# Optimization experiments

Measured on AMD Instinct MI355X. Metric: run time of the kernel, lower is better.

Reference implementation:

```python
import jax, jax.numpy as jnp
import numpy as np

N_NODES = 40000
N_EDGES = 640000
IN_CH = 128
HID_CH = 128
BN_EPS = 1e-5


def setup_inputs() -> dict:
    key = jax.random.key(0)
    k_x, k_ei, k_w, k_g = jax.random.split(key, 4)
    x = jax.random.normal(k_x, (N_NODES, IN_CH), dtype=jnp.float32)
    edge_index = jax.random.randint(k_ei, (2, N_EDGES), 0, N_NODES, dtype=jnp.int32)
    # Glorot init for GCNConv weight, zero bias (PyG defaults)
    limit = float(np.sqrt(6.0 / (IN_CH + HID_CH)))
    W = jax.random.uniform(k_w, (IN_CH, HID_CH), dtype=jnp.float32, minval=-limit, maxval=limit)
    b = jnp.zeros((HID_CH,), dtype=jnp.float32)
    gamma = jnp.ones((HID_CH,), dtype=jnp.float32)
    beta = jnp.zeros((HID_CH,), dtype=jnp.float32)
    return {"x": x, "edge_index": edge_index, "W": W, "b": b, "gamma": gamma, "beta": beta}


def reference(x, edge_index, W, b, gamma, beta):
    N = x.shape[0]
    src, dst = edge_index[0], edge_index[1]

    # --- GCNConv: h = x @ W, symmetric-normalized aggregation with self-loops ---
    h = x @ W  # [N, H]
    ones = jnp.ones((src.shape[0],), dtype=x.dtype)
    deg = jax.ops.segment_sum(ones, dst, num_segments=N) + 1.0  # +1 for self-loop
    dinv = jax.lax.rsqrt(deg)  # deg >= 1 always
    norm = dinv[src] * dinv[dst]  # [E]
    msg = h[src] * norm[:, None]  # [E, H] gather
    agg = jax.ops.segment_sum(msg, dst, num_segments=N)  # scatter-add
    agg = agg + h * (dinv * dinv)[:, None]  # self-loop contribution
    out = agg + b  # bias added after aggregation (PyG GCNConv)

    # --- BatchNorm1d (training mode: batch stats, biased variance) ---
    mean = jnp.mean(out, axis=0)
    var = jnp.mean((out - mean) ** 2, axis=0)
    out = gamma * (out - mean) * jax.lax.rsqrt(var + BN_EPS) + beta

    # --- ReLU (dropout is a no-op in eval) ---
    return jax.nn.relu(out)
```

## Files before the change

### kernel.cpp

```cpp
#include <hip/hip_runtime.h>

#define N_NODES 40000
#define N_EDGES 640000
#define CH 128
#define BN_EPS 1e-5f
#define CAP 64
#define MM_ROWS 32
#define MM_BLOCKS (N_NODES / MM_ROWS)
#define FILL_BLOCKS ((N_EDGES + 255) / 256)


__device__ __forceinline__ float bf_lo(unsigned u) { return __uint_as_float(u << 16); }
__device__ __forceinline__ float bf_hi(unsigned u) { return __uint_as_float(u & 0xffff0000u); }
__device__ __forceinline__ unsigned short f2bf(float f) {
    unsigned u = __float_as_uint(f);
    unsigned r = 0x7fffu + ((u >> 16) & 1u);
    return (unsigned short)((u + r) >> 16);
}
__device__ __forceinline__ unsigned pack2bf(float a, float b) {
    return (unsigned)f2bf(a) | ((unsigned)f2bf(b) << 16);
}

__global__ __launch_bounds__(256) void mm_fill_kernel(const float* __restrict__ x,
                                                      const float* __restrict__ W,
                                                      unsigned short* __restrict__ hbf,
                                                      const int* __restrict__ src,
                                                      const int* __restrict__ dst,
                                                      int* __restrict__ cnt,
                                                      unsigned short* __restrict__ bucket16) {
    __shared__ unsigned Wsb[CH * CH / 2];
    __shared__ unsigned xsb[CH * 16];
    int t = threadIdx.x;
    int bb = blockIdx.x;
    if (bb % 3 != 0) {
        int fillIdx = bb - (bb / 3) - 1;
        int base = cnt[N_NODES];
        int e = fillIdx * 256 + t;
        if (e < N_EDGES) {
            int d = dst[e];
            int slot = atomicAdd(&cnt[d], 1) - base;
            if (slot < CAP) bucket16[d * CAP + slot] = (unsigned short)src[e];
        }
        return;
    }
    int mmIdx = bb / 3;
    for (int i = t; i < CH * CH / 4; i += 256) {
        float4 w = ((const float4*)W)[i];
        uint2 p;
        p.x = pack2bf(w.x, w.y);
        p.y = pack2bf(w.z, w.w);
        ((uint2*)Wsb)[i] = p;
    }
    size_t row0 = (size_t)mmIdx * MM_ROWS;
    {
        int p = t >> 4;
        int k4a = t & 15;
#pragma unroll
        for (int kk = 0; kk < 2; ++kk) {
            int k4 = k4a + kk * 16;
            float4 xa = ((const float4*)(x + (row0 + p) * CH))[k4];
            float4 xb = ((const float4*)(x + (row0 + p + 16) * CH))[k4];
            xsb[(k4 * 4 + 0) * 16 + p] = pack2bf(xa.x, xb.x);
            xsb[(k4 * 4 + 1) * 16 + p] = pack2bf(xa.y, xb.y);
            xsb[(k4 * 4 + 2) * 16 + p] = pack2bf(xa.z, xb.z);
            xsb[(k4 * 4 + 3) * 16 + p] = pack2bf(xa.w, xb.w);
        }
    }
    __syncthreads();
    int ch4 = t & 31;
    int rg = t >> 5;
    float4 accA = {0,0,0,0}, accB = {0,0,0,0}, accC = {0,0,0,0}, accD = {0,0,0,0};
#pragma unroll 8
    for (int k = 0; k < CH; ++k) {
        uint2 wp = ((const uint2*)Wsb)[k * 32 + ch4];
        unsigned xpa = xsb[k * 16 + rg];
        unsigned xpb = xsb[k * 16 + rg + 8];
        float w0 = bf_lo(wp.x), w1 = bf_hi(wp.x), w2 = bf_lo(wp.y), w3 = bf_hi(wp.y);
        float xa0 = bf_lo(xpa), xa1 = bf_hi(xpa);
        float xb0 = bf_lo(xpb), xb1 = bf_hi(xpb);
        accA.x += xa0 * w0; accA.y += xa0 * w1; accA.z += xa0 * w2; accA.w += xa0 * w3;
        accB.x += xa1 * w0; accB.y += xa1 * w1; accB.z += xa1 * w2; accB.w += xa1 * w3;
        accC.x += xb0 * w0; accC.y += xb0 * w1; accC.z += xb0 * w2; accC.w += xb0 * w3;
        accD.x += xb1 * w0; accD.y += xb1 * w1; accD.z += xb1 * w2; accD.w += xb1 * w3;
    }
    uint2 o;
    o.x = pack2bf(accA.x, accA.y); o.y = pack2bf(accA.z, accA.w);
    ((uint2*)(hbf + (row0 + rg) * CH))[ch4] = o;
    o.x = pack2bf(accB.x, accB.y); o.y = pack2bf(accB.z, accB.w);
    ((uint2*)(hbf + (row0 + rg + 16) * CH))[ch4] = o;
    o.x = pack2bf(accC.x, accC.y); o.y = pack2bf(accC.z, accC.w);
    ((uint2*)(hbf + (row0 + rg + 8) * CH))[ch4] = o;
    o.x = pack2bf(accD.x, accD.y); o.y = pack2bf(accD.z, accD.w);
    ((uint2*)(hbf + (row0 + rg + 24) * CH))[ch4] = o;
}

__global__ __launch_bounds__(256) void aggregate_kernel(const unsigned short* __restrict__ bucket16,
                                                        const int* __restrict__ cnt,
                                                        const unsigned short* __restrict__ hbf,
                                                        const float* __restrict__ b,
                                                        float* __restrict__ out,
                                                        float* __restrict__ sums32) {
    __shared__ float bsum[CH], bsq[CH];
    int t = threadIdx.x;
    if (t < CH) { bsum[t] = 0.0f; bsq[t] = 0.0f; }
    __syncthreads();
    int base = cnt[N_NODES];
    int n = blockIdx.x * 4 + (t >> 6);
    int lane = t & 63;
    int quarter = lane >> 4;
    int ql = lane & 15;
    int cn = cnt[n] - base;
    int m = cn < CAP ? cn : CAP;
    float dn = rsqrtf((float)cn + 1.0f);
    const uint4* h4 = (const uint4*)hbf;
    unsigned sx_pre = (lane < m) ? (unsigned)bucket16[n * CAP + lane] : 0u;
    float a0 = 0, a1 = 0, a2 = 0, a3 = 0, a4 = 0, a5 = 0, a6 = 0, a7 = 0;
    for (int jj = 0; jj < m; jj += 16) {
        int e = jj + quarter * 4;
        unsigned sx0 = (unsigned)__shfl((int)sx_pre, e, 64);
        unsigned sx1 = (unsigned)__shfl((int)sx_pre, e + 1, 64);
        unsigned sx2 = (unsigned)__shfl((int)sx_pre, e + 2, 64);
        unsigned sx3 = (unsigned)__shfl((int)sx_pre, e + 3, 64);
        int c0g = cnt[sx0];
        int c1g = cnt[sx1];
        int c2g = cnt[sx2];
        int c3g = cnt[sx3];
        uint4 r0 = h4[(size_t)sx0 * 16 + ql];
        uint4 r1 = h4[(size_t)sx1 * 16 + ql];
        uint4 r2 = h4[(size_t)sx2 * 16 + ql];
        uint4 r3 = h4[(size_t)sx3 * 16 + ql];
        float d0 = (e     < m) ? rsqrtf((float)(c0g - base) + 1.0f) : 0.0f;
        float d1 = (e + 1 < m) ? rsqrtf((float)(c1g - base) + 1.0f) : 0.0f;
        float d2 = (e + 2 < m) ? rsqrtf((float)(c2g - base) + 1.0f) : 0.0f;
        float d3 = (e + 3 < m) ? rsqrtf((float)(c3g - base) + 1.0f) : 0.0f;
        a0 += bf_lo(r0.x) * d0; a1 += bf_hi(r0.x) * d0;
        a2 += bf_lo(r0.y) * d0; a3 += bf_hi(r0.y) * d0;
        a4 += bf_lo(r0.z) * d0; a5 += bf_hi(r0.z) * d0;
        a6 += bf_lo(r0.w) * d0; a7 += bf_hi(r0.w) * d0;
        a0 += bf_lo(r1.x) * d1; a1 += bf_hi(r1.x) * d1;
        a2 += bf_lo(r1.y) * d1; a3 += bf_hi(r1.y) * d1;
        a4 += bf_lo(r1.z) * d1; a5 += bf_hi(r1.z) * d1;
        a6 += bf_lo(r1.w) * d1; a7 += bf_hi(r1.w) * d1;
        a0 += bf_lo(r2.x) * d2; a1 += bf_hi(r2.x) * d2;
        a2 += bf_lo(r2.y) * d2; a3 += bf_hi(r2.y) * d2;
        a4 += bf_lo(r2.z) * d2; a5 += bf_hi(r2.z) * d2;
        a6 += bf_lo(r2.w) * d2; a7 += bf_hi(r2.w) * d2;
        a0 += bf_lo(r3.x) * d3; a1 += bf_hi(r3.x) * d3;
        a2 += bf_lo(r3.y) * d3; a3 += bf_hi(r3.y) * d3;
        a4 += bf_lo(r3.z) * d3; a5 += bf_hi(r3.z) * d3;
        a6 += bf_lo(r3.w) * d3; a7 += bf_hi(r3.w) * d3;
    }
    a0 += __shfl_xor(a0, 16, 64); a0 += __shfl_xor(a0, 32, 64);
    a1 += __shfl_xor(a1, 16, 64); a1 += __shfl_xor(a1, 32, 64);
    a2 += __shfl_xor(a2, 16, 64); a2 += __shfl_xor(a2, 32, 64);
    a3 += __shfl_xor(a3, 16, 64); a3 += __shfl_xor(a3, 32, 64);
    a4 += __shfl_xor(a4, 16, 64); a4 += __shfl_xor(a4, 32, 64);
    a5 += __shfl_xor(a5, 16, 64); a5 += __shfl_xor(a5, 32, 64);
    a6 += __shfl_xor(a6, 16, 64); a6 += __shfl_xor(a6, 32, 64);
    a7 += __shfl_xor(a7, 16, 64); a7 += __shfl_xor(a7, 32, 64);
    if (quarter == 0) {
        uint4 raw = h4[(size_t)n * 16 + ql];
        float s2 = dn * dn;
        float4 bv0 = ((const float4*)b)[ql * 2];
        float4 bv1 = ((const float4*)b)[ql * 2 + 1];
        float o0 = a0 * dn + bf_lo(raw.x) * s2 + bv0.x;
        float o1 = a1 * dn + bf_hi(raw.x) * s2 + bv0.y;
        float o2 = a2 * dn + bf_lo(raw.y) * s2 + bv0.z;
        float o3 = a3 * dn + bf_hi(raw.y) * s2 + bv0.w;
        float o4 = a4 * dn + bf_lo(raw.z) * s2 + bv1.x;
        float o5 = a5 * dn + bf_hi(raw.z) * s2 + bv1.y;
        float o6 = a6 * dn + bf_lo(raw.w) * s2 + bv1.z;
        float o7 = a7 * dn + bf_hi(raw.w) * s2 + bv1.w;
        float4* op = (float4*)(out + (size_t)n * CH + ql * 8);
        float4 w0 = {o0, o1, o2, o3};
        float4 w1 = {o4, o5, o6, o7};
        op[0] = w0;
        op[1] = w1;
        int c0 = ql * 8;
        atomicAdd(&bsum[c0 + 0], o0); atomicAdd(&bsq[c0 + 0], o0 * o0);
        atomicAdd(&bsum[c0 + 1], o1); atomicAdd(&bsq[c0 + 1], o1 * o1);
        atomicAdd(&bsum[c0 + 2], o2); atomicAdd(&bsq[c0 + 2], o2 * o2);
        atomicAdd(&bsum[c0 + 3], o3); atomicAdd(&bsq[c0 + 3], o3 * o3);
        atomicAdd(&bsum[c0 + 4], o4); atomicAdd(&bsq[c0 + 4], o4 * o4);
        atomicAdd(&bsum[c0 + 5], o5); atomicAdd(&bsq[c0 + 5], o5 * o5);
        atomicAdd(&bsum[c0 + 6], o6); atomicAdd(&bsq[c0 + 6], o6 * o6);
        atomicAdd(&bsum[c0 + 7], o7); atomicAdd(&bsq[c0 + 7], o7 * o7);
    }
    __syncthreads();
    atomicAdd(&sums32[(blockIdx.x & 31) * 256 + t], (t < CH) ? bsum[t] : bsq[t - CH]);
}

__global__ __launch_bounds__(256) void bn_relu_kernel(float* __restrict__ out,
                                                      const float* __restrict__ sums32,
                                                      const float* __restrict__ gamma,
                                                      const float* __restrict__ beta) {
    __shared__ float sc[CH], sh[CH];
    int t = threadIdx.x;
    if (t < CH) {
        float P = sums32[32 * 256];
        float s = -32.0f * P, q = -32.0f * P;
#pragma unroll
        for (int k = 0; k < 32; ++k) {
            s += sums32[k * 256 + t];
            q += sums32[k * 256 + CH + t];
        }
        const float invN = 1.0f / (float)N_NODES;
        float mean = s * invN;
        float var = q * invN - mean * mean;
        float scale = gamma[t] * rsqrtf(var + BN_EPS);
        sc[t] = scale;
        sh[t] = beta[t] - mean * scale;
    }
    __syncthreads();
    int i = blockIdx.x * 256 + t;
    int c0 = (i & 31) * 4;
    float4 v = ((float4*)out)[i];
    float r0 = v.x * sc[c0] + sh[c0];
    float r1 = v.y * sc[c0 + 1] + sh[c0 + 1];
    float r2 = v.z * sc[c0 + 2] + sh[c0 + 2];
    float r3 = v.w * sc[c0 + 3] + sh[c0 + 3];
    v.x = r0 > 0.0f ? r0 : 0.0f;
    v.y = r1 > 0.0f ? r1 : 0.0f;
    v.z = r2 > 0.0f ? r2 : 0.0f;
    v.w = r3 > 0.0f ? r3 : 0.0f;
    ((float4*)out)[i] = v;
}

extern "C" void kernel_launch(void* const* d_in, const int* in_sizes, int n_in,
                              void* d_out, int out_size, void* d_ws, size_t ws_size,
                              hipStream_t stream) {
    const float* x = (const float*)d_in[0];
    const int* ei = (const int*)d_in[1];
    const float* W = (const float*)d_in[2];
    const float* b = (const float*)d_in[3];
    const float* gamma = (const float*)d_in[4];
    const float* beta = (const float*)d_in[5];
    float* out = (float*)d_out;
    const int* src = ei;
    const int* dst = ei + N_EDGES;
    char* ws = (char*)d_ws;

    unsigned short* hbf = (unsigned short*)ws;
    int* cnt = (int*)(ws + 10240000);
    float* sums32 = (float*)(ws + 10400256);
    unsigned short* bucket16 = (unsigned short*)(ws + 10433280);

    mm_fill_kernel<<<MM_BLOCKS + FILL_BLOCKS, 256, 0, stream>>>(x, W, hbf, src, dst, cnt,
                                                                bucket16);
    aggregate_kernel<<<N_NODES / 4, 256, 0, stream>>>(bucket16, cnt, hbf, b, out, sums32);
    bn_relu_kernel<<<N_NODES * CH / 4 / 256, 256, 0, stream>>>(out, sums32, gamma, beta);
}
```

Baseline: 197.1 us.

## Process four nodes per wavefront in aggregation with staged coalesced output

Each wavefront in the aggregate kernel now handles four destination nodes instead of one. It interleaves their neighbor gathers to raise memory-level parallelism and reduces the per-block shared-memory atomics by first summing across quarters with shuffles. Outputs are staged in shared memory and written back as coalesced float4 rows, and the grid shrinks to N/16 blocks. In exchange, register pressure rises from the 4x8 accumulators and the 16 in-flight row loads, which may lower occupancy. The loop trip count is also set by the largest degree of the four nodes, so lanes can diverge.

Result: slower. 201.6 us (+2.2%).

```diff
diff --git a/kernel.cpp b/kernel.cpp
--- a/kernel.cpp
+++ b/kernel.cpp
@@ -101,92 +101,138 @@
                                                         float* __restrict__ out,
                                                         float* __restrict__ sums32) {
     __shared__ float bsum[CH], bsq[CH];
+    __shared__ float ostage[16][CH + 4];
     int t = threadIdx.x;
     if (t < CH) { bsum[t] = 0.0f; bsq[t] = 0.0f; }
     __syncthreads();
     int base = cnt[N_NODES];
-    int n = blockIdx.x * 4 + (t >> 6);
+    int wid = t >> 6;
     int lane = t & 63;
     int quarter = lane >> 4;
     int ql = lane & 15;
-    int cn = cnt[n] - base;
-    int m = cn < CAP ? cn : CAP;
-    float dn = rsqrtf((float)cn + 1.0f);
+    int n0 = (blockIdx.x * 4 + wid) * 4;
     const uint4* h4 = (const uint4*)hbf;
-    unsigned sx_pre = (lane < m) ? (unsigned)bucket16[n * CAP + lane] : 0u;
-    float a0 = 0, a1 = 0, a2 = 0, a3 = 0, a4 = 0, a5 = 0, a6 = 0, a7 = 0;
-    for (int jj = 0; jj < m; jj += 16) {
-        int e = jj + quarter * 4;
-        unsigned sx0 = (unsigned)__shfl((int)sx_pre, e, 64);
-        unsigned sx1 = (unsigned)__shfl((int)sx_pre, e + 1, 64);
-        unsigned sx2 = (unsigned)__shfl((int)sx_pre, e + 2, 64);
-        unsigned sx3 = (unsigned)__shfl((int)sx_pre, e + 3, 64);
-        int c0g = cnt[sx0];
-        int c1g = cnt[sx1];
-        int c2g = cnt[sx2];
-        int c3g = cnt[sx3];
-        uint4 r0 = h4[(size_t)sx0 * 16 + ql];
-        uint4 r1 = h4[(size_t)sx1 * 16 + ql];
-        uint4 r2 = h4[(size_t)sx2 * 16 + ql];
-        uint4 r3 = h4[(size_t)sx3 * 16 + ql];
-        float d0 = (e     < m) ? rsqrtf((float)(c0g - base) + 1.0f) : 0.0f;
-        float d1 = (e + 1 < m) ? rsqrtf((float)(c1g - base) + 1.0f) : 0.0f;
-        float d2 = (e + 2 < m) ? rsqrtf((float)(c2g - base) + 1.0f) : 0.0f;
-        float d3 = (e + 3 < m) ? rsqrtf((float)(c3g - base) + 1.0f) : 0.0f;
-        a0 += bf_lo(r0.x) * d0; a1 += bf_hi(r0.x) * d0;
-        a2 += bf_lo(r0.y) * d0; a3 += bf_hi(r0.y) * d0;
-        a4 += bf_lo(r0.z) * d0; a5 += bf_hi(r0.z) * d0;
-        a6 += bf_lo(r0.w) * d0; a7 += bf_hi(r0.w) * d0;
-        a0 += bf_lo(r1.x) * d1; a1 += bf_hi(r1.x) * d1;
-        a2 += bf_lo(r1.y) * d1; a3 += bf_hi(r1.y) * d1;
-        a4 += bf_lo(r1.z) * d1; a5 += bf_hi(r1.z) * d1;
-        a6 += bf_lo(r1.w) * d1; a7 += bf_hi(r1.w) * d1;
-        a0 += bf_lo(r2.x) * d2; a1 += bf_hi(r2.x) * d2;
-        a2 += bf_lo(r2.y) * d2; a3 += bf_hi(r2.y) * d2;
-        a4 += bf_lo(r2.z) * d2; a5 += bf_hi(r2.z) * d2;
-        a6 += bf_lo(r2.w) * d2; a7 += bf_hi(r2.w) * d2;
-        a0 += bf_lo(r3.x) * d3; a1 += bf_hi(r3.x) * d3;
-        a2 += bf_lo(r3.y) * d3; a3 += bf_hi(r3.y) * d3;
-        a4 += bf_lo(r3.z) * d3; a5 += bf_hi(r3.z) * d3;
-        a6 += bf_lo(r3.w) * d3; a7 += bf_hi(r3.w) * d3;
-    }
-    a0 += __shfl_xor(a0, 16, 64); a0 += __shfl_xor(a0, 32, 64);
-    a1 += __shfl_xor(a1, 16, 64); a1 += __shfl_xor(a1, 32, 64);
-    a2 += __shfl_xor(a2, 16, 64); a2 += __shfl_xor(a2, 32, 64);
-    a3 += __shfl_xor(a3, 16, 64); a3 += __shfl_xor(a3, 32, 64);
-    a4 += __shfl_xor(a4, 16, 64); a4 += __shfl_xor(a4, 32, 64);
-    a5 += __shfl_xor(a5, 16, 64); a5 += __shfl_xor(a5, 32, 64);
-    a6 += __shfl_xor(a6, 16, 64); a6 += __shfl_xor(a6, 32, 64);
-    a7 += __shfl_xor(a7, 16, 64); a7 += __shfl_xor(a7, 32, 64);
-    if (quarter == 0) {
-        uint4 raw = h4[(size_t)n * 16 + ql];
-        float s2 = dn * dn;
-        float4 bv0 = ((const float4*)b)[ql * 2];
-        float4 bv1 = ((const float4*)b)[ql * 2 + 1];
-        float o0 = a0 * dn + bf_lo(raw.x) * s2 + bv0.x;
-        float o1 = a1 * dn + bf_hi(raw.x) * s2 + bv0.y;
-        float o2 = a2 * dn + bf_lo(raw.y) * s2 + bv0.z;
-        float o3 = a3 * dn + bf_hi(raw.y) * s2 + bv0.w;
-        float o4 = a4 * dn + bf_lo(raw.z) * s2 + bv1.x;
-        float o5 = a5 * dn + bf_hi(raw.z) * s2 + bv1.y;
-        float o6 = a6 * dn + bf_lo(raw.w) * s2 + bv1.z;
-        float o7 = a7 * dn + bf_hi(raw.w) * s2 + bv1.w;
-        float4* op = (float4*)(out + (size_t)n * CH + ql * 8);
-        float4 w0 = {o0, o1, o2, o3};
-        float4 w1 = {o4, o5, o6, o7};
-        op[0] = w0;
-        op[1] = w1;
-        int c0 = ql * 8;
-        atomicAdd(&bsum[c0 + 0], o0); atomicAdd(&bsq[c0 + 0], o0 * o0);
-        atomicAdd(&bsum[c0 + 1], o1); atomicAdd(&bsq[c0 + 1], o1 * o1);
-        atomicAdd(&bsum[c0 + 2], o2); atomicAdd(&bsq[c0 + 2], o2 * o2);
-        atomicAdd(&bsum[c0 + 3], o3); atomicAdd(&bsq[c0 + 3], o3 * o3);
-        atomicAdd(&bsum[c0 + 4], o4); atomicAdd(&bsq[c0 + 4], o4 * o4);
-        atomicAdd(&bsum[c0 + 5], o5); atomicAdd(&bsq[c0 + 5], o5 * o5);
-        atomicAdd(&bsum[c0 + 6], o6); atomicAdd(&bsq[c0 + 6], o6 * o6);
-        atomicAdd(&bsum[c0 + 7], o7); atomicAdd(&bsq[c0 + 7], o7 * o7);
-    }
-    __syncthreads();
+
+    int4 cn4 = *(const int4*)(cnt + n0);
+    uint4 self = h4[(size_t)(n0 + quarter) * 16 + ql];
+    unsigned sp[4];
+    sp[0] = (unsigned)bucket16[(n0 + 0) * CAP + lane];
+    sp[1] = (unsigned)bucket16[(n0 + 1) * CAP + lane];
+    sp[2] = (unsigned)bucket16[(n0 + 2) * CAP + lane];
+    sp[3] = (unsigned)bucket16[(n0 + 3) * CAP + lane];
+
+    int c[4] = {cn4.x - base, cn4.y - base, cn4.z - base, cn4.w - base};
+    int m[4];
+    float dnv[4];
+#pragma unroll
+    for (int i = 0; i < 4; ++i) {
+        m[i] = c[i] < CAP ? c[i] : CAP;
+        dnv[i] = rsqrtf((float)c[i] + 1.0f);
+        sp[i] = (lane < m[i]) ? sp[i] : 0u;
+    }
+    int mmax = max(max(m[0], m[1]), max(m[2], m[3]));
+
+    float acc[4][8];
+#pragma unroll
+    for (int i = 0; i < 4; ++i)
+#pragma unroll
+        for (int k = 0; k < 8; ++k) acc[i][k] = 0.0f;
+
+    int e0 = quarter * 4;
+    for (int jj = 0; jj < mmax; jj += 16) {
+        int e = jj + e0;
+        uint4 r[4][4];
+        int cg[4][4];
+#pragma unroll
+        for (int i = 0; i < 4; ++i) {
+            if (jj < m[i]) {
+                int s0 = __shfl((int)sp[i], e, 64);
+                int s1 = __shfl((int)sp[i], e + 1, 64);
+                int s2 = __shfl((int)sp[i], e + 2, 64);
+                int s3 = __shfl((int)sp[i], e + 3, 64);
+                cg[i][0] = cnt[s0]; cg[i][1] = cnt[s1];
+                cg[i][2] = cnt[s2]; cg[i][3] = cnt[s3];
+                r[i][0] = h4[(size_t)s0 * 16 + ql];
+                r[i][1] = h4[(size_t)s1 * 16 + ql];
+                r[i][2] = h4[(size_t)s2 * 16 + ql];
+                r[i][3] = h4[(size_t)s3 * 16 + ql];
+            }
+        }
+#pragma unroll
+        for (int i = 0; i < 4; ++i) {
+            if (jj < m[i]) {
+#pragma unroll
+                for (int k = 0; k < 4; ++k) {
+                    float d = (e + k < m[i]) ? rsqrtf((float)(cg[i][k] - base) + 1.0f) : 0.0f;
+                    uint4 rv = r[i][k];
+                    acc[i][0] += bf_lo(rv.x) * d; acc[i][1] += bf_hi(rv.x) * d;
+                    acc[i][2] += bf_lo(rv.y) * d; acc[i][3] += bf_hi(rv.y) * d;
+                    acc[i][4] += bf_lo(rv.z) * d; acc[i][5] += bf_hi(rv.z) * d;
+                    acc[i][6] += bf_lo(rv.w) * d; acc[i][7] += bf_hi(rv.w) * d;
+                }
+            }
+        }
+    }
+
+#pragma unroll
+    for (int i = 0; i < 4; ++i)
+#pragma unroll
+        for (int k = 0; k < 8; ++k) {
+            float v = acc[i][k];
+            v += __shfl_xor(v, 16, 64);
+            v += __shfl_xor(v, 32, 64);
+            acc[i][k] = v;
+        }
+
+    float dn = (quarter & 2) ? ((quarter & 1) ? dnv[3] : dnv[2])
+                             : ((quarter & 1) ? dnv[1] : dnv[0]);
+    float s2 = dn * dn;
+    float4 bv0 = ((const float4*)b)[ql * 2];
+    float4 bv1 = ((const float4*)b)[ql * 2 + 1];
+    float o[8];
+#pragma unroll
+    for (int k = 0; k < 8; ++k) {
+        float v01 = (quarter & 1) ? acc[1][k] : acc[0][k];
+        float v23 = (quarter & 1) ? acc[3][k] : acc[2][k];
+        o[k] = ((quarter & 2) ? v23 : v01) * dn;
+    }
+    o[0] += bf_lo(self.x) * s2 + bv0.x;
+    o[1] += bf_hi(self.x) * s2 + bv0.y;
+    o[2] += bf_lo(self.y) * s2 + bv0.z;
+    o[3] += bf_hi(self.y) * s2 + bv0.w;
+    o[4] += bf_lo(self.z) * s2 + bv1.x;
+    o[5] += bf_hi(self.z) * s2 + bv1.y;
+    o[6] += bf_lo(self.w) * s2 + bv1.z;
+    o[7] += bf_hi(self.w) * s2 + bv1.w;
+
+    int ni = wid * 4 + quarter;
+    float4 w0 = {o[0], o[1], o[2], o[3]};
+    float4 w1 = {o[4], o[5], o[6], o[7]};
+    *(float4*)&ostage[ni][ql * 8] = w0;
+    *(float4*)&ostage[ni][ql * 8 + 4] = w1;
+
+#pragma unroll
+    for (int k = 0; k < 8; ++k) {
+        float s = o[k];
+        float q2 = o[k] * o[k];
+        s += __shfl_xor(s, 16, 64); s += __shfl_xor(s, 32, 64);
+        q2 += __shfl_xor(q2, 16, 64); q2 += __shfl_xor(q2, 32, 64);
+        if (quarter == 0) {
+            atomicAdd(&bsum[ql * 8 + k], s);
+            atomicAdd(&bsq[ql * 8 + k], q2);
+        }
+    }
+    __syncthreads();
+
+    {
+        size_t blk0 = (size_t)blockIdx.x * 16;
+        int j0 = t, r0 = j0 >> 5, f0 = j0 & 31;
+        float4 va = *(float4*)&ostage[r0][f0 * 4];
+        ((float4*)(out + (blk0 + r0) * CH))[f0] = va;
+        int j1 = t + 256, r1 = j1 >> 5, f1 = j1 & 31;
+        float4 vb = *(float4*)&ostage[r1][f1 * 4];
+        ((float4*)(out + (blk0 + r1) * CH))[f1] = vb;
+    }
     atomicAdd(&sums32[(blockIdx.x & 31) * 256 + t], (t < CH) ? bsum[t] : bsq[t - CH]);
 }
 
@@ -247,6 +293,6 @@
 
     mm_fill_kernel<<<MM_BLOCKS + FILL_BLOCKS, 256, 0, stream>>>(x, W, hbf, src, dst, cnt,
                                                                 bucket16);
-    aggregate_kernel<<<N_NODES / 4, 256, 0, stream>>>(bucket16, cnt, hbf, b, out, sums32);
+    aggregate_kernel<<<N_NODES / 16, 256, 0, stream>>>(bucket16, cnt, hbf, b, out, sums32);
     bn_relu_kernel<<<N_NODES * CH / 4 / 256, 256, 0, stream>>>(out, sums32, gamma, beta);
 }
```

## Coarsen aggregation to four nodes per wave and vectorize bucket fill

Applied to the files above, without the earlier changes.

The aggregate kernel now has each wave process four nodes in sequence, so the grid is a quarter of its former size. It keeps per-thread BN sum and sum-of-squares partials in registers and issues LDS and global atomics once per block instead of per node, cutting atomic traffic and block launch overhead. The fill path now handles four edges per thread using int4 loads, and the block interleave changes to two matmul blocks per fill block. The costs are less parallelism to hide gather latency and serialized per-node work within each wave.

New measurement: 167.0 us. 15.3% less time.

```diff
diff --git a/kernel.cpp b/kernel.cpp
--- a/kernel.cpp
+++ b/kernel.cpp
@@ -7,7 +7,7 @@
 #define CAP 64
 #define MM_ROWS 32
 #define MM_BLOCKS (N_NODES / MM_ROWS)
-#define FILL_BLOCKS ((N_EDGES + 255) / 256)
+#define FILL_BLOCKS (N_EDGES / 1024)
 
 
 __device__ __forceinline__ float bf_lo(unsigned u) { return __uint_as_float(u << 16); }
@@ -32,18 +32,21 @@
     __shared__ unsigned xsb[CH * 16];
     int t = threadIdx.x;
     int bb = blockIdx.x;
-    if (bb % 3 != 0) {
-        int fillIdx = bb - (bb / 3) - 1;
+    if (bb % 3 == 2) {
+        int fi = bb / 3;
         int base = cnt[N_NODES];
-        int e = fillIdx * 256 + t;
-        if (e < N_EDGES) {
-            int d = dst[e];
-            int slot = atomicAdd(&cnt[d], 1) - base;
-            if (slot < CAP) bucket16[d * CAP + slot] = (unsigned short)src[e];
+        int4 dd = ((const int4*)dst)[fi * 256 + t];
+        int4 ss = ((const int4*)src)[fi * 256 + t];
+        int d[4] = {dd.x, dd.y, dd.z, dd.w};
+        int s[4] = {ss.x, ss.y, ss.z, ss.w};
+#pragma unroll
+        for (int k = 0; k < 4; ++k) {
+            int slot = atomicAdd(&cnt[d[k]], 1) - base;
+            if (slot < CAP) bucket16[d[k] * CAP + slot] = (unsigned short)s[k];
         }
         return;
     }
-    int mmIdx = bb / 3;
+    int mmIdx = (bb / 3) * 2 + (bb % 3);
     for (int i = t; i < CH * CH / 4; i += 256) {
         float4 w = ((const float4*)W)[i];
         uint2 p;
@@ -105,86 +108,103 @@
     if (t < CH) { bsum[t] = 0.0f; bsq[t] = 0.0f; }
     __syncthreads();
     int base = cnt[N_NODES];
-    int n = blockIdx.x * 4 + (t >> 6);
+    int wid = t >> 6;
     int lane = t & 63;
     int quarter = lane >> 4;
     int ql = lane & 15;
-    int cn = cnt[n] - base;
-    int m = cn < CAP ? cn : CAP;
-    float dn = rsqrtf((float)cn + 1.0f);
     const uint4* h4 = (const uint4*)hbf;
-    unsigned sx_pre = (lane < m) ? (unsigned)bucket16[n * CAP + lane] : 0u;
-    float a0 = 0, a1 = 0, a2 = 0, a3 = 0, a4 = 0, a5 = 0, a6 = 0, a7 = 0;
-    for (int jj = 0; jj < m; jj += 16) {
-        int e = jj + quarter * 4;
-        unsigned sx0 = (unsigned)__shfl((int)sx_pre, e, 64);
-        unsigned sx1 = (unsigned)__shfl((int)sx_pre, e + 1, 64);
-        unsigned sx2 = (unsigned)__shfl((int)sx_pre, e + 2, 64);
-        unsigned sx3 = (unsigned)__shfl((int)sx_pre, e + 3, 64);
-        int c0g = cnt[sx0];
-        int c1g = cnt[sx1];
-        int c2g = cnt[sx2];
-        int c3g = cnt[sx3];
-        uint4 r0 = h4[(size_t)sx0 * 16 + ql];
-        uint4 r1 = h4[(size_t)sx1 * 16 + ql];
-        uint4 r2 = h4[(size_t)sx2 * 16 + ql];
-        uint4 r3 = h4[(size_t)sx3 * 16 + ql];
-        float d0 = (e     < m) ? rsqrtf((float)(c0g - base) + 1.0f) : 0.0f;
-        float d1 = (e + 1 < m) ? rsqrtf((float)(c1g - base) + 1.0f) : 0.0f;
-        float d2 = (e + 2 < m) ? rsqrtf((float)(c2g - base) + 1.0f) : 0.0f;
-        float d3 = (e + 3 < m) ? rsqrtf((float)(c3g - base) + 1.0f) : 0.0f;
-        a0 += bf_lo(r0.x) * d0; a1 += bf_hi(r0.x) * d0;
-        a2 += bf_lo(r0.y) * d0; a3 += bf_hi(r0.y) * d0;
-        a4 += bf_lo(r0.z) * d0; a5 += bf_hi(r0.z) * d0;
-        a6 += bf_lo(r0.w) * d0; a7 += bf_hi(r0.w) * d0;
-        a0 += bf_lo(r1.x) * d1; a1 += bf_hi(r1.x) * d1;
-        a2 += bf_lo(r1.y) * d1; a3 += bf_hi(r1.y) * d1;
-        a4 += bf_lo(r1.z) * d1; a5 += bf_hi(r1.z) * d1;
-        a6 += bf_lo(r1.w) * d1; a7 += bf_hi(r1.w) * d1;
-        a0 += bf_lo(r2.x) * d2; a1 += bf_hi(r2.x) * d2;
-        a2 += bf_lo(r2.y) * d2; a3 += bf_hi(r2.y) * d2;
-        a4 += bf_lo(r2.z) * d2; a5 += bf_hi(r2.z) * d2;
-        a6 += bf_lo(r2.w) * d2; a7 += bf_hi(r2.w) * d2;
-        a0 += bf_lo(r3.x) * d3; a1 += bf_hi(r3.x) * d3;
-        a2 += bf_lo(r3.y) * d3; a3 += bf_hi(r3.y) * d3;
-        a4 += bf_lo(r3.z) * d3; a5 += bf_hi(r3.z) * d3;
-        a6 += bf_lo(r3.w) * d3; a7 += bf_hi(r3.w) * d3;
-    }
-    a0 += __shfl_xor(a0, 16, 64); a0 += __shfl_xor(a0, 32, 64);
-    a1 += __shfl_xor(a1, 16, 64); a1 += __shfl_xor(a1, 32, 64);
-    a2 += __shfl_xor(a2, 16, 64); a2 += __shfl_xor(a2, 32, 64);
-    a3 += __shfl_xor(a3, 16, 64); a3 += __shfl_xor(a3, 32, 64);
-    a4 += __shfl_xor(a4, 16, 64); a4 += __shfl_xor(a4, 32, 64);
-    a5 += __shfl_xor(a5, 16, 64); a5 += __shfl_xor(a5, 32, 64);
-    a6 += __shfl_xor(a6, 16, 64); a6 += __shfl_xor(a6, 32, 64);
-    a7 += __shfl_xor(a7, 16, 64); a7 += __shfl_xor(a7, 32, 64);
+    float4 bv0 = ((const float4*)b)[ql * 2];
+    float4 bv1 = ((const float4*)b)[ql * 2 + 1];
+    int n_base = blockIdx.x * 16 + wid * 4;
+    float s0 = 0, s1 = 0, s2 = 0, s3 = 0, s4 = 0, s5 = 0, s6 = 0, s7 = 0;
+    float q0 = 0, q1 = 0, q2 = 0, q3 = 0, q4 = 0, q5 = 0, q6 = 0, q7 = 0;
+#pragma unroll 1
+    for (int it = 0; it < 4; ++it) {
+        int n = n_base + it;
+        int cn = cnt[n] - base;
+        int m = cn < CAP ? cn : CAP;
+        float dn = rsqrtf((float)cn + 1.0f);
+        unsigned sx_pre = (lane < m) ? (unsigned)bucket16[n * CAP + lane] : 0u;
+        float a0 = 0, a1 = 0, a2 = 0, a3 = 0, a4 = 0, a5 = 0, a6 = 0, a7 = 0;
+        for (int jj = 0; jj < m; jj += 16) {
+            int e = jj + quarter * 4;
+            unsigned sx0 = (unsigned)__shfl((int)sx_pre, e, 64);
+            unsigned sx1 = (unsigned)__shfl((int)sx_pre, e + 1, 64);
+            unsigned sx2 = (unsigned)__shfl((int)sx_pre, e + 2, 64);
+            unsigned sx3 = (unsigned)__shfl((int)sx_pre, e + 3, 64);
+            int c0g = cnt[sx0];
+            int c1g = cnt[sx1];
+            int c2g = cnt[sx2];
+            int c3g = cnt[sx3];
+            uint4 r0 = h4[(size_t)sx0 * 16 + ql];
+            uint4 r1 = h4[(size_t)sx1 * 16 + ql];
+            uint4 r2 = h4[(size_t)sx2 * 16 + ql];
+            uint4 r3 = h4[(size_t)sx3 * 16 + ql];
+            float d0 = (e     < m) ? rsqrtf((float)(c0g - base) + 1.0f) : 0.0f;
+            float d1 = (e + 1 < m) ? rsqrtf((float)(c1g - base) + 1.0f) : 0.0f;
+            float d2 = (e + 2 < m) ? rsqrtf((float)(c2g - base) + 1.0f) : 0.0f;
+            float d3 = (e + 3 < m) ? rsqrtf((float)(c3g - base) + 1.0f) : 0.0f;
+            a0 += bf_lo(r0.x) * d0; a1 += bf_hi(r0.x) * d0;
+            a2 += bf_lo(r0.y) * d0; a3 += bf_hi(r0.y) * d0;
+            a4 += bf_lo(r0.z) * d0; a5 += bf_hi(r0.z) * d0;
+            a6 += bf_lo(r0.w) * d0; a7 += bf_hi(r0.w) * d0;
+            a0 += bf_lo(r1.x) * d1; a1 += bf_hi(r1.x) * d1;
+            a2 += bf_lo(r1.y) * d1; a3 += bf_hi(r1.y) * d1;
+            a4 += bf_lo(r1.z) * d1; a5 += bf_hi(r1.z) * d1;
+            a6 += bf_lo(r1.w) * d1; a7 += bf_hi(r1.w) * d1;
+            a0 += bf_lo(r2.x) * d2; a1 += bf_hi(r2.x) * d2;
+            a2 += bf_lo(r2.y) * d2; a3 += bf_hi(r2.y) * d2;
+            a4 += bf_lo(r2.z) * d2; a5 += bf_hi(r2.z) * d2;
+            a6 += bf_lo(r2.w) * d2; a7 += bf_hi(r2.w) * d2;
+            a0 += bf_lo(r3.x) * d3; a1 += bf_hi(r3.x) * d3;
+            a2 += bf_lo(r3.y) * d3; a3 += bf_hi(r3.y) * d3;
+            a4 += bf_lo(r3.z) * d3; a5 += bf_hi(r3.z) * d3;
+            a6 += bf_lo(r3.w) * d3; a7 += bf_hi(r3.w) * d3;
+        }
+        a0 += __shfl_xor(a0, 16, 64); a0 += __shfl_xor(a0, 32, 64);
+        a1 += __shfl_xor(a1, 16, 64); a1 += __shfl_xor(a1, 32, 64);
+        a2 += __shfl_xor(a2, 16, 64); a2 += __shfl_xor(a2, 32, 64);
+        a3 += __shfl_xor(a3, 16, 64); a3 += __shfl_xor(a3, 32, 64);
+        a4 += __shfl_xor(a4, 16, 64); a4 += __shfl_xor(a4, 32, 64);
+        a5 += __shfl_xor(a5, 16, 64); a5 += __shfl_xor(a5, 32, 64);
+        a6 += __shfl_xor(a6, 16, 64); a6 += __shfl_xor(a6, 32, 64);
+        a7 += __shfl_xor(a7, 16, 64); a7 += __shfl_xor(a7, 32, 64);
+        if (quarter == 0) {
+            uint4 raw = h4[(size_t)n * 16 + ql];
+            float sq = dn * dn;
+            float o0 = a0 * dn + bf_lo(raw.x) * sq + bv0.x;
+            float o1 = a1 * dn + bf_hi(raw.x) * sq + bv0.y;
+            float o2 = a2 * dn + bf_lo(raw.y) * sq + bv0.z;
+            float o3 = a3 * dn + bf_hi(raw.y) * sq + bv0.w;
+            float o4 = a4 * dn + bf_lo(raw.z) * sq + bv1.x;
+            float o5 = a5 * dn + bf_hi(raw.z) * sq + bv1.y;
+            float o6 = a6 * dn + bf_lo(raw.w) * sq + bv1.z;
+            float o7 = a7 * dn + bf_hi(raw.w) * sq + bv1.w;
+            float4* op = (float4*)(out + (size_t)n * CH + ql * 8);
+            float4 w0 = {o0, o1, o2, o3};
+            float4 w1 = {o4, o5, o6, o7};
+            op[0] = w0;
+            op[1] = w1;
+            s0 += o0; q0 += o0 * o0;
+            s1 += o1; q1 += o1 * o1;
+            s2 += o2; q2 += o2 * o2;
+            s3 += o3; q3 += o3 * o3;
+            s4 += o4; q4 += o4 * o4;
+            s5 += o5; q5 += o5 * o5;
+            s6 += o6; q6 += o6 * o6;
+            s7 += o7; q7 += o7 * o7;
+        }
+    }
     if (quarter == 0) {
-        uint4 raw = h4[(size_t)n * 16 + ql];
-        float s2 = dn * dn;
-        float4 bv0 = ((const float4*)b)[ql * 2];
-        float4 bv1 = ((const float4*)b)[ql * 2 + 1];
-        float o0 = a0 * dn + bf_lo(raw.x) * s2 + bv0.x;
-        float o1 = a1 * dn + bf_hi(raw.x) * s2 + bv0.y;
-        float o2 = a2 * dn + bf_lo(raw.y) * s2 + bv0.z;
-        float o3 = a3 * dn + bf_hi(raw.y) * s2 + bv0.w;
-        float o4 = a4 * dn + bf_lo(raw.z) * s2 + bv1.x;
-        float o5 = a5 * dn + bf_hi(raw.z) * s2 + bv1.y;
-        float o6 = a6 * dn + bf_lo(raw.w) * s2 + bv1.z;
-        float o7 = a7 * dn + bf_hi(raw.w) * s2 + bv1.w;
-        float4* op = (float4*)(out + (size_t)n * CH + ql * 8);
-        float4 w0 = {o0, o1, o2, o3};
-        float4 w1 = {o4, o5, o6, o7};
-        op[0] = w0;
-        op[1] = w1;
         int c0 = ql * 8;
-        atomicAdd(&bsum[c0 + 0], o0); atomicAdd(&bsq[c0 + 0], o0 * o0);
-        atomicAdd(&bsum[c0 + 1], o1); atomicAdd(&bsq[c0 + 1], o1 * o1);
-        atomicAdd(&bsum[c0 + 2], o2); atomicAdd(&bsq[c0 + 2], o2 * o2);
-        atomicAdd(&bsum[c0 + 3], o3); atomicAdd(&bsq[c0 + 3], o3 * o3);
-        atomicAdd(&bsum[c0 + 4], o4); atomicAdd(&bsq[c0 + 4], o4 * o4);
-        atomicAdd(&bsum[c0 + 5], o5); atomicAdd(&bsq[c0 + 5], o5 * o5);
-        atomicAdd(&bsum[c0 + 6], o6); atomicAdd(&bsq[c0 + 6], o6 * o6);
-        atomicAdd(&bsum[c0 + 7], o7); atomicAdd(&bsq[c0 + 7], o7 * o7);
+        atomicAdd(&bsum[c0 + 0], s0); atomicAdd(&bsq[c0 + 0], q0);
+        atomicAdd(&bsum[c0 + 1], s1); atomicAdd(&bsq[c0 + 1], q1);
+        atomicAdd(&bsum[c0 + 2], s2); atomicAdd(&bsq[c0 + 2], q2);
+        atomicAdd(&bsum[c0 + 3], s3); atomicAdd(&bsq[c0 + 3], q3);
+        atomicAdd(&bsum[c0 + 4], s4); atomicAdd(&bsq[c0 + 4], q4);
+        atomicAdd(&bsum[c0 + 5], s5); atomicAdd(&bsq[c0 + 5], q5);
+        atomicAdd(&bsum[c0 + 6], s6); atomicAdd(&bsq[c0 + 6], q6);
+        atomicAdd(&bsum[c0 + 7], s7); atomicAdd(&bsq[c0 + 7], q7);
     }
     __syncthreads();
     atomicAdd(&sums32[(blockIdx.x & 31) * 256 + t], (t < CH) ? bsum[t] : bsq[t - CH]);
@@ -247,6 +267,6 @@
 
     mm_fill_kernel<<<MM_BLOCKS + FILL_BLOCKS, 256, 0, stream>>>(x, W, hbf, src, dst, cnt,
                                                                 bucket16);
-    aggregate_kernel<<<N_NODES / 4, 256, 0, stream>>>(bucket16, cnt, hbf, b, out, sums32);
+    aggregate_kernel<<<N_NODES / 16, 256, 0, stream>>>(bucket16, cnt, hbf, b, out, sums32);
     bn_relu_kernel<<<N_NODES * CH / 4 / 256, 256, 0, stream>>>(out, sums32, gamma, beta);
 }
```
